# Kernel optimization log

Measured on AMD Instinct MI355X. Metric: run time of the kernel, lower is better.

## Reference

```python
import jax, jax.numpy as jnp
import numpy as np
from jax import lax

H = 512      # hidden_size (== embed dim)
K = 128      # attr_size
V = 32000    # output_size (vocab)
ANUM = 20    # aspect_num = len(aspect_ids)//100
N, B = 64, 32
T, S, A = 256, 32, 5


def setup_inputs() -> dict:
    key = jax.random.key(0)
    ks = jax.random.split(key, 32)
    f = lambda i, shape, s=0.02: (jax.random.normal(ks[i], shape, jnp.float32) * s)
    inp = {
        "input_seq": jax.random.randint(ks[0], (N, B), 0, V, jnp.int32),
        "last_hidden": jax.random.normal(ks[1], (1, B, H), jnp.float32),
        "encoder_out1": jax.random.normal(ks[2], (T, B, H), jnp.float32),
        "encoder_out2": jax.random.normal(ks[3], (S, B, H), jnp.float32),
        "encoder_out3": jax.random.normal(ks[4], (A, B, K), jnp.float32),
        "encoder_out4": jax.random.normal(ks[5], (A, B, ANUM), jnp.float32),
        "aspect_ids": jax.random.randint(ks[6], (100 * ANUM,), 0, V, jnp.int32),
        # learned parameters
        "emb": f(7, (V, H)),
        "gru_Wih": f(8, (3 * H, H)), "gru_Whh": f(9, (3 * H, H)),
        "gru_bih": f(10, (3 * H,)), "gru_bhh": f(11, (3 * H,)),
        "attn_W": f(12, (H, 2 * H)), "attn_b": f(13, (H,)), "attn_v": f(14, (H,)),
        "attr_W": f(15, (H, H + K)), "attr_b": f(16, (H,)), "attr_v": f(17, (H,)),
        "concat_W": f(18, (H, 3 * H + K)), "concat_b": f(19, (H,)),
        "out_W": f(20, (V, H)), "out_b": f(21, (V,)),
        "gate_W": f(22, (ANUM, 2 * H + ANUM)), "gate_b": f(23, (ANUM,)),
        "proj_W": f(24, (ANUM, 2 * ANUM)), "proj_b": f(25, (ANUM,)),
    }
    return inp


def _gru(x, h0, Wih, Whh, bih, bhh):
    # x: (N,B,H); h0: (B,H). PyTorch gate order: reset, update, new.
    def step(h, xt):
        gi = xt @ Wih.T + bih
        gh = h @ Whh.T + bhh
        ir, iz, inn = jnp.split(gi, 3, axis=-1)
        hr, hz, hn = jnp.split(gh, 3, axis=-1)
        r = jax.nn.sigmoid(ir + hr)
        z = jax.nn.sigmoid(iz + hz)
        n = jnp.tanh(inn + r * hn)
        h_new = (1.0 - z) * n + z * h
        return h_new, h_new
    hT, ys = lax.scan(step, h0, x)
    return ys, hT


def _attn(hidden, enc, W, b, v):
    # Faithful to Attn/AttributeAttn: energies[b,n,t] = tanh(v . (W @ cat(hidden[n,b], enc[t,b]) + b))
    # W @ cat = hidden @ Wh^T + enc @ We^T; dot with v distributes -> avoid (T,N,B,*) blowup.
    Hh = hidden.shape[-1]
    Wh, We = W[:, :Hh], W[:, Hh:]
    a = hidden @ (Wh.T @ v) + jnp.dot(b, v)   # (N,B)
    c = enc @ (We.T @ v)                       # (T,B)
    e = jnp.tanh(a.T[:, :, None] + c.T[:, None, :])  # (B,N,T)
    return jax.nn.softmax(e, axis=2)


def reference(input_seq, last_hidden, encoder_out1, encoder_out2, encoder_out3,
              encoder_out4, aspect_ids, emb, gru_Wih, gru_Whh, gru_bih, gru_bhh,
              attn_W, attn_b, attn_v, attr_W, attr_b, attr_v, concat_W, concat_b,
              out_W, out_b, gate_W, gate_b, proj_W, proj_b):
    seq_len = input_seq.shape[0]
    embedded = emb[input_seq]                                   # (N,B,H), dropout=eval noop
    rnn_output, hT = _gru(embedded, last_hidden[0], gru_Wih, gru_Whh, gru_bih, gru_bhh)
    hidden = hT[None]                                           # (1,B,H)

    aw1 = _attn(rnn_output, encoder_out1, attn_W, attn_b, attn_v)   # (B,N,T)
    ctx1 = jnp.einsum('bnt,tbh->nbh', aw1, encoder_out1)
    aw2 = _attn(rnn_output, encoder_out2, attn_W, attn_b, attn_v)   # (B,N,S)
    ctx2 = jnp.einsum('bns,sbh->nbh', aw2, encoder_out2)
    aw3 = _attn(rnn_output, encoder_out3, attr_W, attr_b, attr_v)   # (B,N,A)
    ctx3 = jnp.einsum('bna,abk->nbk', aw3, encoder_out3)

    concat_input = jnp.concatenate([rnn_output, ctx1, ctx2, ctx3], axis=2)
    concat_output = jnp.tanh(concat_input @ concat_W.T + concat_b)  # (N,B,H)
    output = concat_output @ out_W.T + out_b                        # (N,B,V)

    e4 = jnp.concatenate([encoder_out4[0], encoder_out4[1]], axis=-1)  # (B,2*ANUM)
    e4 = e4 @ proj_W.T + proj_b                                        # (B,ANUM)
    e4 = jnp.broadcast_to(e4[None], (seq_len,) + e4.shape)             # (N,B,ANUM)

    gate = jnp.tanh(jnp.concatenate([embedded, rnn_output, e4], axis=2) @ gate_W.T + gate_b)
    vals = jnp.tile(gate, (1, 1, 100))                                 # (N,B,100*ANUM)
    output = output.at[:, :, aspect_ids].add(vals)
    return output, hidden, aw1, aw2, aw3, gate
```

## Files before the change

### kernel.cpp

```cpp
#include <hip/hip_runtime.h>
#include <hip/hip_bf16.h>

#define HDIM 512
#define KA   128
#define VOC  32000
#define ANUMC 20
#define NSEQ 64
#define BATCH 32
#define TLEN 256
#define SLEN 32
#define ALEN 5
#define NB   2048
#define CIN  1664
#define G3H  1536
#define GB   64

typedef __bf16 bf16;
typedef bf16 v8bf __attribute__((ext_vector_type(8)));
typedef float v4f __attribute__((ext_vector_type(4)));

#define DEV __device__ __forceinline__

DEV float sigmoidf_(float x) { return 1.f / (1.f + expf(-x)); }

__global__ void k_tick(unsigned* ctr) {
  if (threadIdx.x == 0) ++*ctr;
}

__global__ void k_vec(const float* __restrict__ attn_W, const float* __restrict__ attn_b,
                      const float* __restrict__ attn_v,
                      const float* __restrict__ attr_W, const float* __restrict__ attr_b,
                      const float* __restrict__ attr_v,
                      const float* __restrict__ enc4, const float* __restrict__ pW,
                      const float* __restrict__ pb, float* __restrict__ misc) {
  int tid = threadIdx.x;
  int blk = blockIdx.x;
  if (blk == 0) {
    for (int i = tid; i < 512; i += 256) {
      float s = 0.f;
      for (int j = 0; j < 512; ++j) s += attn_W[j * 1024 + i] * attn_v[j];
      misc[i] = s;
    }
  } else if (blk == 1) {
    for (int i = tid; i < 512; i += 256) {
      float s = 0.f;
      for (int j = 0; j < 512; ++j) s += attn_W[j * 1024 + 512 + i] * attn_v[j];
      misc[512 + i] = s;
    }
  } else if (blk == 2) {
    for (int i = tid; i < 512; i += 256) {
      float s = 0.f;
      for (int j = 0; j < 512; ++j) s += attr_W[j * 640 + i] * attr_v[j];
      misc[1024 + i] = s;
    }
  } else {
    for (int i = tid; i < 128; i += 256) {
      float s = 0.f;
      for (int j = 0; j < 512; ++j) s += attr_W[j * 640 + 512 + i] * attr_v[j];
      misc[1536 + i] = s;
    }
    if (tid == 128) {
      float s = 0.f;
      for (int j = 0; j < 512; ++j) s += attn_b[j] * attn_v[j];
      misc[1664] = s;
    }
    if (tid == 129) {
      float s = 0.f;
      for (int j = 0; j < 512; ++j) s += attr_b[j] * attr_v[j];
      misc[1665] = s;
    }
    for (int i = tid; i < BATCH * ANUMC; i += 256) {
      int b = i / ANUMC, j = i % ANUMC;
      float s = pb[j];
      for (int q = 0; q < ANUMC; ++q) s += pW[j * 40 + q] * enc4[b * ANUMC + q];
      for (int q = 0; q < ANUMC; ++q) s += pW[j * 40 + 20 + q] * enc4[BATCH * ANUMC + b * ANUMC + q];
      misc[1792 + i] = s;
    }
  }
}

__global__ void k_embcvt(const int* __restrict__ seq, const float* __restrict__ emb,
                         float* __restrict__ embedded, bf16* __restrict__ emb_bf,
                         const float* __restrict__ Wih, bf16* __restrict__ Wih_bf,
                         const float* __restrict__ cW, bf16* __restrict__ cW_bf,
                         const float* __restrict__ oW, bf16* __restrict__ oW_bf) {
  size_t i = (size_t)blockIdx.x * 256 + threadIdx.x;
  const size_t s0 = 1048576, s1 = s0 + 786432, s2 = s1 + 851968, s3 = s2 + 16384000;
  if (i < s0) {
    int row = (int)(i >> 9), col = (int)(i & 511);
    float v = emb[(size_t)seq[row] * 512 + col];
    embedded[i] = v;
    emb_bf[i] = (bf16)v;
  } else if (i < s1) {
    size_t j = i - s0;
    Wih_bf[j] = (bf16)Wih[j];
  } else if (i < s2) {
    size_t j = i - s1;
    cW_bf[j] = (bf16)cW[j];
  } else if (i < s3) {
    size_t j = i - s2;
    oW_bf[j] = (bf16)oW[j];
  }
}

__global__ void k_c(const float* __restrict__ enc1, const float* __restrict__ enc2,
                    const float* __restrict__ enc3, float* __restrict__ misc) {
  int i = blockIdx.x * 256 + threadIdx.x;
  const float* u1e = misc + 512;
  const float* u3e = misc + 1536;
  if (i < 8192) {
    const float* row = enc1 + (size_t)i * 512;
    float s = 0.f;
#pragma unroll 4
    for (int j = 0; j < 512; j += 4) {
      float4 a = *(const float4*)(row + j);
      float4 u = *(const float4*)(u1e + j);
      s += a.x * u.x + a.y * u.y + a.z * u.z + a.w * u.w;
    }
    misc[2560 + i] = s;
  } else if (i < 8192 + 1024) {
    int k = i - 8192;
    const float* row = enc2 + (size_t)k * 512;
    float s = 0.f;
#pragma unroll 4
    for (int j = 0; j < 512; j += 4) {
      float4 a = *(const float4*)(row + j);
      float4 u = *(const float4*)(u1e + j);
      s += a.x * u.x + a.y * u.y + a.z * u.z + a.w * u.w;
    }
    misc[10752 + k] = s;
  } else if (i < 8192 + 1024 + 160) {
    int k = i - 9216;
    const float* row = enc3 + (size_t)k * 128;
    float s = 0.f;
#pragma unroll 4
    for (int j = 0; j < 128; j += 4) {
      float4 a = *(const float4*)(row + j);
      float4 u = *(const float4*)(u3e + j);
      s += a.x * u.x + a.y * u.y + a.z * u.z + a.w * u.w;
    }
    misc[11776 + k] = s;
  }
}

template <int EPI>
__global__ __launch_bounds__(256) void k_gemm_bt(const bf16* __restrict__ A,
                                                 const bf16* __restrict__ Bm,
                                                 const float* __restrict__ bias,
                                                 float* __restrict__ Cf, bf16* __restrict__ Cb,
                                                 int M, int Nn, int Kd) {
  __shared__ __align__(16) unsigned short As[128 * 64];
  __shared__ __align__(16) unsigned short Bs[128 * 64];
  int tid = threadIdx.x;
  int m0 = blockIdx.y * 128;
  int n0 = blockIdx.x * 128;
  int lane = tid & 63;
  int wv = tid >> 6;
  int wm = wv & 1, wn = wv >> 1;
  int l15 = lane & 15, quad = lane >> 4;
  int srow = tid >> 3;
  int sch = tid & 7;

  v4f acc[4][4];
#pragma unroll
  for (int i = 0; i < 4; ++i)
#pragma unroll
    for (int j = 0; j < 4; ++j) acc[i][j] = (v4f){0.f, 0.f, 0.f, 0.f};

  for (int kb = 0; kb < Kd; kb += 64) {
#pragma unroll
    for (int r = 0; r < 4; ++r) {
      int row = r * 32 + srow;
      uint4 va = *(const uint4*)(A + (size_t)(m0 + row) * Kd + kb + sch * 8);
      *(uint4*)((char*)As + row * 128 + ((sch ^ (row & 7)) << 4)) = va;
      uint4 vb = *(const uint4*)(Bm + (size_t)(n0 + row) * Kd + kb + sch * 8);
      *(uint4*)((char*)Bs + row * 128 + ((sch ^ (row & 7)) << 4)) = vb;
    }
    __syncthreads();
#pragma unroll
    for (int ks = 0; ks < 2; ++ks) {
      v8bf af[4], bfr[4];
      int c = ks * 4 + quad;
#pragma unroll
      for (int i = 0; i < 4; ++i) {
        int mr = wm * 64 + i * 16 + l15;
        af[i] = *(const v8bf*)((const char*)As + mr * 128 + ((c ^ (mr & 7)) << 4));
      }
#pragma unroll
      for (int j = 0; j < 4; ++j) {
        int nr = wn * 64 + j * 16 + l15;
        bfr[j] = *(const v8bf*)((const char*)Bs + nr * 128 + ((c ^ (nr & 7)) << 4));
      }
#pragma unroll
      for (int i = 0; i < 4; ++i)
#pragma unroll
        for (int j = 0; j < 4; ++j)
          acc[i][j] = __builtin_amdgcn_mfma_f32_16x16x32_bf16(af[i], bfr[j], acc[i][j], 0, 0, 0);
    }
    __syncthreads();
  }
#pragma unroll
  for (int i = 0; i < 4; ++i) {
    int gr0 = m0 + wm * 64 + i * 16 + quad * 4;
#pragma unroll
    for (int j = 0; j < 4; ++j) {
      int gc = n0 + wn * 64 + j * 16 + l15;
      float bs = bias[gc];
#pragma unroll
      for (int reg = 0; reg < 4; ++reg) {
        float v = acc[i][j][reg] + bs;
        if (EPI == 1)
          Cb[(size_t)(gr0 + reg) * Nn + gc] = (bf16)tanhf(v);
        else
          Cf[(size_t)(gr0 + reg) * Nn + gc] = v;
      }
    }
  }
}

__global__ __launch_bounds__(256) void k_gru(const float* __restrict__ gi,
                                             const float* __restrict__ Whh,
                                             const float* __restrict__ bhh,
                                             const float* __restrict__ lasth,
                                             float* __restrict__ rnn,
                                             bf16* __restrict__ concat_bf,
                                             unsigned long long* __restrict__ hx,
                                             const unsigned* __restrict__ ctr) {
  struct SMEM {
    unsigned short whh[24 * 512];
    unsigned short hs[32 * 512];
    float gh[32 * 29];
    unsigned short hnew[256];
  };
  __shared__ __align__(16) SMEM sm;
  int tid = threadIdx.x;
  int blk = blockIdx.x;
  int c0 = blk * 8;
  unsigned tagbase = (*ctr) << 6;

  for (int idx = tid; idx < 24 * 64; idx += 256) {
    int row = idx >> 6, cc = idx & 63;
    int g = row >> 3, jj = row & 7;
    const float* src = Whh + (size_t)(g * 512 + c0 + jj) * 512 + cc * 8;
    float4 x = *(const float4*)src;
    float4 y = *(const float4*)(src + 4);
    v8bf vv;
    vv[0] = (bf16)x.x; vv[1] = (bf16)x.y; vv[2] = (bf16)x.z; vv[3] = (bf16)x.w;
    vv[4] = (bf16)y.x; vv[5] = (bf16)y.y; vv[6] = (bf16)y.z; vv[7] = (bf16)y.w;
    *(v8bf*)((char*)sm.whh + row * 1024 + ((cc ^ (row & 7)) << 4)) = vv;
  }

  int lane = tid & 63;
  int w = tid >> 6;
  int l15 = lane & 15, quad = lane >> 4;
  int m0 = (w & 1) * 16;
  int n0 = (w >> 1) * 16;

  int cb = tid >> 3, j = tid & 7, c = c0 + j;
  float hprev = lasth[cb * 512 + c];
  float b_r = bhh[c], b_z = bhh[512 + c], b_n = bhh[1024 + c];

  for (int t = 0; t < 64; ++t) {
    const float* gii = gi + ((size_t)t * 32 + cb) * G3H;
    float g_r = gii[c];
    float g_z = gii[512 + c];
    float g_n = gii[1024 + c];

    if (t == 0) {
#pragma unroll
      for (int rnd = 0; rnd < 8; ++rnd) {
        int ch = rnd * 256 + tid;
        int bb = ch >> 6, cc = ch & 63;
        const float* hp = lasth + bb * 512 + cc * 8;
        float4 x = *(const float4*)hp;
        float4 y = *(const float4*)(hp + 4);
        v8bf vv;
        vv[0] = (bf16)x.x; vv[1] = (bf16)x.y; vv[2] = (bf16)x.z; vv[3] = (bf16)x.w;
        vv[4] = (bf16)y.x; vv[5] = (bf16)y.y; vv[6] = (bf16)y.z; vv[7] = (bf16)y.w;
        *(v8bf*)((char*)sm.hs + bb * 1024 + ((cc ^ (bb & 7)) << 4)) = vv;
      }
    } else {
      unsigned tg = tagbase + (unsigned)t;
      const unsigned long long* src = hx + (size_t)(t & 1) * 8192 + tid;
      unsigned long long v[32];
#pragma unroll
      for (int i = 0; i < 32; ++i)
        v[i] = __hip_atomic_load(src + i * 256, __ATOMIC_RELAXED, __HIP_MEMORY_SCOPE_AGENT);
      for (;;) {
        unsigned stale = 0u;
#pragma unroll
        for (int i = 0; i < 32; ++i)
          if ((unsigned)(v[i] >> 32) != tg) stale |= (1u << i);
        if (!stale) break;
        __builtin_amdgcn_s_sleep(1);
#pragma unroll
        for (int i = 0; i < 32; ++i)
          if (stale & (1u << i))
            v[i] = __hip_atomic_load(src + i * 256, __ATOMIC_RELAXED, __HIP_MEMORY_SCOPE_AGENT);
      }
      int cc = tid >> 2, b4 = (tid & 3) * 4;
#pragma unroll
      for (int i = 0; i < 32; ++i)
        *(unsigned*)((char*)sm.hs + i * 1024 + (((cc ^ (i & 7)) << 4) | b4)) = (unsigned)v[i];
    }
    __syncthreads();

    {
      v4f acc0 = (v4f){0.f, 0.f, 0.f, 0.f};
      v4f acc1 = (v4f){0.f, 0.f, 0.f, 0.f};
      int mr = m0 + l15;
      int nr = n0 + l15;
#pragma unroll
      for (int it = 0; it < 8; ++it) {
        {
          int ccx = it * 4 + quad;
          v8bf af = *(const v8bf*)((const char*)sm.hs + mr * 1024 + ((ccx ^ (mr & 7)) << 4));
          v8bf bfr = *(const v8bf*)((const char*)sm.whh + nr * 1024 + ((ccx ^ (nr & 7)) << 4));
          acc0 = __builtin_amdgcn_mfma_f32_16x16x32_bf16(af, bfr, acc0, 0, 0, 0);
        }
        {
          int ccx = (it + 8) * 4 + quad;
          v8bf af = *(const v8bf*)((const char*)sm.hs + mr * 1024 + ((ccx ^ (mr & 7)) << 4));
          v8bf bfr = *(const v8bf*)((const char*)sm.whh + nr * 1024 + ((ccx ^ (nr & 7)) << 4));
          acc1 = __builtin_amdgcn_mfma_f32_16x16x32_bf16(af, bfr, acc1, 0, 0, 0);
        }
      }
      v4f acc = acc0 + acc1;
      if (n0 == 0 || l15 < 8) {
#pragma unroll
        for (int reg = 0; reg < 4; ++reg)
          sm.gh[(m0 + quad * 4 + reg) * 29 + n0 + l15] = acc[reg];
      }
    }
    __syncthreads();

    {
      float ar = sm.gh[cb * 29 + j] + b_r;
      float az = sm.gh[cb * 29 + 8 + j] + b_z;
      float an = sm.gh[cb * 29 + 16 + j] + b_n;
      float rg = sigmoidf_(g_r + ar);
      float zg = sigmoidf_(g_z + az);
      float ng = tanhf(g_n + rg * an);
      float hn = (1.f - zg) * ng + zg * hprev;
      hprev = hn;
      rnn[((size_t)t * 32 + cb) * 512 + c] = hn;
      bf16 hb = (bf16)hn;
      concat_bf[((size_t)t * 32 + cb) * CIN + c] = hb;
      sm.hnew[tid] = *(unsigned short*)&hb;
    }

    if (t < 63) {
      __syncthreads();
      if (tid < 128) {
        int cbq = tid >> 2, wj = tid & 3;
        const unsigned short* hp = sm.hnew + cbq * 8 + wj * 2;
        unsigned long long pk = (unsigned long long)hp[0] |
                                ((unsigned long long)hp[1] << 16) |
                                ((unsigned long long)(tagbase + (unsigned)(t + 1)) << 32);
        __hip_atomic_store(hx + (size_t)((t + 1) & 1) * 8192 + cbq * 256 + blk * 4 + wj, pk,
                           __ATOMIC_RELAXED, __HIP_MEMORY_SCOPE_AGENT);
      }
    }
  }
}

__global__ __launch_bounds__(256) void k_attnrow(const float* __restrict__ rnn,
                                                 const float* __restrict__ misc,
                                                 float* __restrict__ aw1,
                                                 float* __restrict__ aw2,
                                                 float* __restrict__ aw3) {
  int wv = (blockIdx.x * 256 + threadIdx.x) >> 6;
  int lane = threadIdx.x & 63;
  if (wv >= 2048) return;
  int n = wv >> 5, b = wv & 31;
  const float* u1a = misc;
  const float* u3h = misc + 1024;
  const float* c1 = misc + 2560;
  const float* c2 = misc + 10752;
  const float* c3 = misc + 11776;
  const float* row = rnn + (size_t)(n * 32 + b) * 512;
  float s1 = 0.f, s3 = 0.f;
#pragma unroll
  for (int q = 0; q < 8; ++q) {
    int j = lane * 8 + q;
    float rv = row[j];
    s1 += rv * u1a[j];
    s3 += rv * u3h[j];
  }
  for (int o = 32; o > 0; o >>= 1) {
    s1 += __shfl_down(s1, o);
    s3 += __shfl_down(s3, o);
  }
  s1 = __shfl(s1, 0) + misc[1664];
  s3 = __shfl(s3, 0) + misc[1665];

  float e[4];
  float mx = -1e30f;
#pragma unroll
  for (int q = 0; q < 4; ++q) {
    int t = q * 64 + lane;
    e[q] = tanhf(s1 + c1[t * 32 + b]);
    mx = fmaxf(mx, e[q]);
  }
  for (int o = 32; o > 0; o >>= 1) mx = fmaxf(mx, __shfl_xor(mx, o));
  float sum = 0.f;
#pragma unroll
  for (int q = 0; q < 4; ++q) {
    e[q] = expf(e[q] - mx);
    sum += e[q];
  }
  for (int o = 32; o > 0; o >>= 1) sum += __shfl_xor(sum, o);
  float inv = 1.f / sum;
  size_t base1 = (size_t)(b * 64 + n) * 256;
#pragma unroll
  for (int q = 0; q < 4; ++q) aw1[base1 + q * 64 + lane] = e[q] * inv;

  float e2 = (lane < 32) ? tanhf(s1 + c2[lane * 32 + b]) : -1e30f;
  float m2 = e2;
  for (int o = 32; o > 0; o >>= 1) m2 = fmaxf(m2, __shfl_xor(m2, o));
  float x2 = (lane < 32) ? expf(e2 - m2) : 0.f;
  float sm2 = x2;
  for (int o = 32; o > 0; o >>= 1) sm2 += __shfl_xor(sm2, o);
  if (lane < 32) aw2[(size_t)(b * 64 + n) * 32 + lane] = x2 / sm2;

  float e3 = (lane < 5) ? tanhf(s3 + c3[lane * 32 + b]) : -1e30f;
  float m3 = e3;
  for (int o = 32; o > 0; o >>= 1) m3 = fmaxf(m3, __shfl_xor(m3, o));
  float x3 = (lane < 5) ? expf(e3 - m3) : 0.f;
  float sm3 = x3;
  for (int o = 32; o > 0; o >>= 1) sm3 += __shfl_xor(sm3, o);
  if (lane < 5) aw3[(size_t)(b * 64 + n) * 5 + lane] = x3 / sm3;
}

template <int TL, int COFF>
__global__ __launch_bounds__(256) void k_ctx(const float* __restrict__ aw,
                                             const float* __restrict__ enc,
                                             bf16* __restrict__ concat_bf) {
  __shared__ __align__(16) float awsT[TL * 36];
  int tid = threadIdx.x;
  int bx = blockIdx.x;
  int b = bx >> 2, q = (bx >> 1) & 1, nh = bx & 1;
  for (int i = tid; i < 32 * TL; i += 256) {
    int n = i / TL, te = i % TL;
    awsT[te * 36 + n] = aw[(size_t)b * 64 * TL + (size_t)(nh * 32 + n) * TL + te];
  }
  __syncthreads();
  int col = q * 256 + tid;
  float4 acc[8];
#pragma unroll
  for (int n4 = 0; n4 < 8; ++n4) acc[n4] = make_float4(0.f, 0.f, 0.f, 0.f);
  for (int te = 0; te < TL; ++te) {
    float v = enc[((size_t)te * 32 + b) * 512 + col];
#pragma unroll
    for (int n4 = 0; n4 < 8; ++n4) {
      float4 wv = *(const float4*)(awsT + te * 36 + n4 * 4);
      acc[n4].x += wv.x * v;
      acc[n4].y += wv.y * v;
      acc[n4].z += wv.z * v;
      acc[n4].w += wv.w * v;
    }
  }
#pragma unroll
  for (int n4 = 0; n4 < 8; ++n4) {
    int ng = nh * 32 + n4 * 4;
    concat_bf[((size_t)(ng + 0) * 32 + b) * CIN + COFF + col] = (bf16)acc[n4].x;
    concat_bf[((size_t)(ng + 1) * 32 + b) * CIN + COFF + col] = (bf16)acc[n4].y;
    concat_bf[((size_t)(ng + 2) * 32 + b) * CIN + COFF + col] = (bf16)acc[n4].z;
    concat_bf[((size_t)(ng + 3) * 32 + b) * CIN + COFF + col] = (bf16)acc[n4].w;
  }
}

__global__ void k_ctx3_misc(const float* __restrict__ aw3, const float* __restrict__ enc3,
                            const float* __restrict__ rnn, bf16* __restrict__ concat_bf,
                            float* __restrict__ hid) {
  int i = blockIdx.x * 256 + threadIdx.x;
  if (i < NB * 128) {
    int row = i >> 7, k = i & 127;
    int n = row >> 5, b = row & 31;
    float s = 0.f;
#pragma unroll
    for (int a = 0; a < 5; ++a)
      s += aw3[(size_t)(b * 64 + n) * 5 + a] * enc3[((size_t)a * 32 + b) * 128 + k];
    concat_bf[(size_t)row * CIN + 1536 + k] = (bf16)s;
  } else {
    int j = i - NB * 128;
    if (j < 16384) hid[j] = rnn[(size_t)63 * 16384 + j];
  }
}

__global__ __launch_bounds__(256) void k_gate(const float* __restrict__ embedded,
                                              const float* __restrict__ rnn,
                                              const float* __restrict__ misc,
                                              const float* __restrict__ gW,
                                              const float* __restrict__ gb,
                                              float* __restrict__ gate) {
  int i = blockIdx.x * 256 + threadIdx.x;
  if (i >= NB * ANUMC) return;
  int row = i / ANUMC, j = i % ANUMC;
  int b = row & 31;
  const float* w = gW + (size_t)j * 1044;
  const float* e = embedded + (size_t)row * 512;
  const float* r = rnn + (size_t)row * 512;
  float s = gb[j];
#pragma unroll 4
  for (int k = 0; k < 512; k += 4) {
    float4 a = *(const float4*)(e + k);
    float4 ww = *(const float4*)(w + k);
    s += a.x * ww.x + a.y * ww.y + a.z * ww.z + a.w * ww.w;
  }
#pragma unroll 4
  for (int k = 0; k < 512; k += 4) {
    float4 a = *(const float4*)(r + k);
    float4 ww = *(const float4*)(w + 512 + k);
    s += a.x * ww.x + a.y * ww.y + a.z * ww.z + a.w * ww.w;
  }
  const float* e4 = misc + 1792 + b * ANUMC;
#pragma unroll
  for (int q = 0; q < ANUMC; ++q) s += w[1024 + q] * e4[q];
  gate[i] = tanhf(s);
}

__global__ __launch_bounds__(256) void k_aspect(const int* __restrict__ ids,
                                                const float* __restrict__ gate,
                                                float* __restrict__ out) {
  __shared__ float gs[ANUMC];
  int row = blockIdx.x;
  if (threadIdx.x < ANUMC) gs[threadIdx.x] = gate[(size_t)row * ANUMC + threadIdx.x];
  __syncthreads();
  float* orow = out + (size_t)row * VOC;
  for (int k = threadIdx.x; k < 2000; k += 256) {
    atomicAdd(orow + ids[k], gs[k % ANUMC]);
  }
}

extern "C" void kernel_launch(void* const* d_in, const int* in_sizes, int n_in,
                              void* d_out, int out_size, void* d_ws, size_t ws_size,
                              hipStream_t stream) {
  const int* seq = (const int*)d_in[0];
  const float* lasth = (const float*)d_in[1];
  const float* enc1 = (const float*)d_in[2];
  const float* enc2 = (const float*)d_in[3];
  const float* enc3 = (const float*)d_in[4];
  const float* enc4 = (const float*)d_in[5];
  const int* aspect = (const int*)d_in[6];
  const float* emb = (const float*)d_in[7];
  const float* Wih = (const float*)d_in[8];
  const float* Whh = (const float*)d_in[9];
  const float* bih = (const float*)d_in[10];
  const float* bhh = (const float*)d_in[11];
  const float* attn_W = (const float*)d_in[12];
  const float* attn_b = (const float*)d_in[13];
  const float* attn_v = (const float*)d_in[14];
  const float* attr_W = (const float*)d_in[15];
  const float* attr_b = (const float*)d_in[16];
  const float* attr_v = (const float*)d_in[17];
  const float* cW = (const float*)d_in[18];
  const float* cbias = (const float*)d_in[19];
  const float* oW = (const float*)d_in[20];
  const float* ob = (const float*)d_in[21];
  const float* gW = (const float*)d_in[22];
  const float* gb = (const float*)d_in[23];
  const float* pW = (const float*)d_in[24];
  const float* pb = (const float*)d_in[25];

  char* ws = (char*)d_ws;
  float* misc = (float*)(ws + 0);
  float* embedded = (float*)(ws + 65536);
  float* gi = (float*)(ws + 4259840);
  float* rnn = (float*)(ws + 16842752);
  bf16* emb_bf = (bf16*)(ws + 21037056);
  bf16* Wih_bf = (bf16*)(ws + 23134208);
  bf16* cW_bf = (bf16*)(ws + 24707072);
  bf16* oW_bf = (bf16*)(ws + 26411008);
  bf16* concat_bf = (bf16*)(ws + 59179008);
  bf16* cout_bf = (bf16*)(ws + 65994752);
  unsigned long long* hx = (unsigned long long*)(ws + 68091904);
  unsigned* ctr = (unsigned*)(misc + 12032);

  float* out = (float*)d_out;
  float* hid_out = out + 65536000;
  float* aw1 = out + 65552384;
  float* aw2 = out + 66076672;
  float* aw3 = out + 66142208;
  float* gate = out + 66152448;

  k_tick<<<1, 64, 0, stream>>>(ctr);
  k_vec<<<4, 256, 0, stream>>>(attn_W, attn_b, attn_v, attr_W, attr_b, attr_v, enc4, pW, pb, misc);
  k_embcvt<<<74496, 256, 0, stream>>>(seq, emb, embedded, emb_bf, Wih, Wih_bf, cW, cW_bf, oW,
                                      oW_bf);
  k_c<<<37, 256, 0, stream>>>(enc1, enc2, enc3, misc);
  k_gemm_bt<0><<<dim3(12, 16), 256, 0, stream>>>(emb_bf, Wih_bf, bih, gi, nullptr, NB, G3H, 512);
  k_gru<<<GB, 256, 0, stream>>>(gi, Whh, bhh, lasth, rnn, concat_bf, hx, ctr);
  k_attnrow<<<512, 256, 0, stream>>>(rnn, misc, aw1, aw2, aw3);
  k_ctx<256, 512><<<128, 256, 0, stream>>>(aw1, enc1, concat_bf);
  k_ctx<32, 1024><<<128, 256, 0, stream>>>(aw2, enc2, concat_bf);
  k_ctx3_misc<<<1088, 256, 0, stream>>>(aw3, enc3, rnn, concat_bf, hid_out);
  k_gate<<<160, 256, 0, stream>>>(embedded, rnn, misc, gW, gb, gate);
  k_gemm_bt<1><<<dim3(4, 16), 256, 0, stream>>>(concat_bf, cW_bf, cbias, nullptr, cout_bf, NB,
                                                512, CIN);
  k_gemm_bt<0><<<dim3(250, 16), 256, 0, stream>>>(cout_bf, oW_bf, ob, out, nullptr, NB, VOC, 512);
  k_aspect<<<2048, 256, 0, stream>>>(aspect, gate, out);
}
```

Baseline: 1.232 ms.

## Fuse aspect scatter into output GEMM epilogue and rework GRU sync

```diff
diff --git a/kernel.cpp b/kernel.cpp
--- a/kernel.cpp
+++ b/kernel.cpp
@@ -23,8 +23,21 @@
 
 DEV float sigmoidf_(float x) { return 1.f / (1.f + expf(-x)); }
 
-__global__ void k_tick(unsigned* ctr) {
-  if (threadIdx.x == 0) ++*ctr;
+__global__ void k_zero(int* bar) {
+  for (int i = threadIdx.x; i < GB * 32; i += 256) bar[i] = 0;
+}
+
+__global__ void k_init0(float* addtab, int* colnz) {
+  int i = blockIdx.x * 256 + threadIdx.x;
+  if (i < VOC * ANUMC) addtab[i] = 0.f;
+  if (i < VOC) colnz[i] = 0;
+}
+__global__ void k_init1(const int* __restrict__ ids, float* addtab, int* colnz) {
+  for (int k = threadIdx.x; k < 2000; k += 256) {
+    int j = ids[k];
+    atomicAdd(addtab + (size_t)j * ANUMC + (k % ANUMC), 1.0f);
+    colnz[j] = 1;
+  }
 }
 
 __global__ void k_vec(const float* __restrict__ attn_W, const float* __restrict__ attn_b,
@@ -148,7 +161,10 @@
                                                  const bf16* __restrict__ Bm,
                                                  const float* __restrict__ bias,
                                                  float* __restrict__ Cf, bf16* __restrict__ Cb,
-                                                 int M, int Nn, int Kd) {
+                                                 int M, int Nn, int Kd,
+                                                 const float* __restrict__ addtab,
+                                                 const int* __restrict__ colnz,
+                                                 const float* __restrict__ gate) {
   __shared__ __align__(16) unsigned short As[128 * 64];
   __shared__ __align__(16) unsigned short Bs[128 * 64];
   int tid = threadIdx.x;
@@ -206,13 +222,32 @@
     for (int j = 0; j < 4; ++j) {
       int gc = n0 + wn * 64 + j * 16 + l15;
       float bs = bias[gc];
-#pragma unroll
-      for (int reg = 0; reg < 4; ++reg) {
-        float v = acc[i][j][reg] + bs;
-        if (EPI == 1)
-          Cb[(size_t)(gr0 + reg) * Nn + gc] = (bf16)tanhf(v);
-        else
+      if (EPI == 2) {
+        int nz = colnz[gc];
+        float ar[ANUMC];
+        if (nz) {
+#pragma unroll
+          for (int a = 0; a < ANUMC; ++a) ar[a] = addtab[(size_t)gc * ANUMC + a];
+        }
+#pragma unroll
+        for (int reg = 0; reg < 4; ++reg) {
+          float v = acc[i][j][reg] + bs;
+          if (nz) {
+            const float* gr = gate + (size_t)(gr0 + reg) * ANUMC;
+#pragma unroll
+            for (int a = 0; a < ANUMC; ++a) v += ar[a] * gr[a];
+          }
           Cf[(size_t)(gr0 + reg) * Nn + gc] = v;
+        }
+      } else {
+#pragma unroll
+        for (int reg = 0; reg < 4; ++reg) {
+          float v = acc[i][j][reg] + bs;
+          if (EPI == 1)
+            Cb[(size_t)(gr0 + reg) * Nn + gc] = (bf16)tanhf(v);
+          else
+            Cf[(size_t)(gr0 + reg) * Nn + gc] = v;
+        }
       }
     }
   }
@@ -225,30 +260,17 @@
                                              float* __restrict__ rnn,
                                              bf16* __restrict__ concat_bf,
                                              unsigned long long* __restrict__ hx,
-                                             const unsigned* __restrict__ ctr) {
+                                             int* __restrict__ bar) {
   struct SMEM {
-    unsigned short whh[24 * 512];
     unsigned short hs[32 * 512];
     float gh[32 * 29];
     unsigned short hnew[256];
+    int go;
   };
   __shared__ __align__(16) SMEM sm;
   int tid = threadIdx.x;
   int blk = blockIdx.x;
   int c0 = blk * 8;
-  unsigned tagbase = (*ctr) << 6;
-
-  for (int idx = tid; idx < 24 * 64; idx += 256) {
-    int row = idx >> 6, cc = idx & 63;
-    int g = row >> 3, jj = row & 7;
-    const float* src = Whh + (size_t)(g * 512 + c0 + jj) * 512 + cc * 8;
-    float4 x = *(const float4*)src;
-    float4 y = *(const float4*)(src + 4);
-    v8bf vv;
-    vv[0] = (bf16)x.x; vv[1] = (bf16)x.y; vv[2] = (bf16)x.z; vv[3] = (bf16)x.w;
-    vv[4] = (bf16)y.x; vv[5] = (bf16)y.y; vv[6] = (bf16)y.z; vv[7] = (bf16)y.w;
-    *(v8bf*)((char*)sm.whh + row * 1024 + ((cc ^ (row & 7)) << 4)) = vv;
-  }
 
   int lane = tid & 63;
   int w = tid >> 6;
@@ -256,9 +278,42 @@
   int m0 = (w & 1) * 16;
   int n0 = (w >> 1) * 16;
 
+  if (tid == 0) sm.go = 0;
+
+  v8bf breg[16];
+  {
+    int nr = n0 + l15;
+    if (nr > 23) nr = 23;
+    const float* wrow = Whh + (size_t)((nr >> 3) * 512 + c0 + (nr & 7)) * 512;
+#pragma unroll
+    for (int it = 0; it < 16; ++it) {
+      int k0 = it * 32 + quad * 8;
+      float4 x = *(const float4*)(wrow + k0);
+      float4 y = *(const float4*)(wrow + k0 + 4);
+      v8bf vv;
+      vv[0] = (bf16)x.x; vv[1] = (bf16)x.y; vv[2] = (bf16)x.z; vv[3] = (bf16)x.w;
+      vv[4] = (bf16)y.x; vv[5] = (bf16)y.y; vv[6] = (bf16)y.z; vv[7] = (bf16)y.w;
+      breg[it] = vv;
+    }
+  }
+
+#pragma unroll
+  for (int rnd = 0; rnd < 8; ++rnd) {
+    int ch = rnd * 256 + tid;
+    int bb = ch >> 6, cc = ch & 63;
+    const float* hp = lasth + bb * 512 + cc * 8;
+    float4 x = *(const float4*)hp;
+    float4 y = *(const float4*)(hp + 4);
+    v8bf vv;
+    vv[0] = (bf16)x.x; vv[1] = (bf16)x.y; vv[2] = (bf16)x.z; vv[3] = (bf16)x.w;
+    vv[4] = (bf16)y.x; vv[5] = (bf16)y.y; vv[6] = (bf16)y.z; vv[7] = (bf16)y.w;
+    *(v8bf*)((char*)sm.hs + bb * 1024 + ((cc ^ (bb & 7)) << 4)) = vv;
+  }
+
   int cb = tid >> 3, j = tid & 7, c = c0 + j;
   float hprev = lasth[cb * 512 + c];
   float b_r = bhh[c], b_z = bhh[512 + c], b_n = bhh[1024 + c];
+  __syncthreads();
 
   for (int t = 0; t < 64; ++t) {
     const float* gii = gi + ((size_t)t * 32 + cb) * G3H;
@@ -266,63 +321,21 @@
     float g_z = gii[512 + c];
     float g_n = gii[1024 + c];
 
-    if (t == 0) {
-#pragma unroll
-      for (int rnd = 0; rnd < 8; ++rnd) {
-        int ch = rnd * 256 + tid;
-        int bb = ch >> 6, cc = ch & 63;
-        const float* hp = lasth + bb * 512 + cc * 8;
-        float4 x = *(const float4*)hp;
-        float4 y = *(const float4*)(hp + 4);
-        v8bf vv;
-        vv[0] = (bf16)x.x; vv[1] = (bf16)x.y; vv[2] = (bf16)x.z; vv[3] = (bf16)x.w;
-        vv[4] = (bf16)y.x; vv[5] = (bf16)y.y; vv[6] = (bf16)y.z; vv[7] = (bf16)y.w;
-        *(v8bf*)((char*)sm.hs + bb * 1024 + ((cc ^ (bb & 7)) << 4)) = vv;
-      }
-    } else {
-      unsigned tg = tagbase + (unsigned)t;
-      const unsigned long long* src = hx + (size_t)(t & 1) * 8192 + tid;
-      unsigned long long v[32];
-#pragma unroll
-      for (int i = 0; i < 32; ++i)
-        v[i] = __hip_atomic_load(src + i * 256, __ATOMIC_RELAXED, __HIP_MEMORY_SCOPE_AGENT);
-      for (;;) {
-        unsigned stale = 0u;
-#pragma unroll
-        for (int i = 0; i < 32; ++i)
-          if ((unsigned)(v[i] >> 32) != tg) stale |= (1u << i);
-        if (!stale) break;
-        __builtin_amdgcn_s_sleep(1);
-#pragma unroll
-        for (int i = 0; i < 32; ++i)
-          if (stale & (1u << i))
-            v[i] = __hip_atomic_load(src + i * 256, __ATOMIC_RELAXED, __HIP_MEMORY_SCOPE_AGENT);
-      }
-      int cc = tid >> 2, b4 = (tid & 3) * 4;
-#pragma unroll
-      for (int i = 0; i < 32; ++i)
-        *(unsigned*)((char*)sm.hs + i * 1024 + (((cc ^ (i & 7)) << 4) | b4)) = (unsigned)v[i];
-    }
-    __syncthreads();
-
     {
       v4f acc0 = (v4f){0.f, 0.f, 0.f, 0.f};
       v4f acc1 = (v4f){0.f, 0.f, 0.f, 0.f};
       int mr = m0 + l15;
-      int nr = n0 + l15;
 #pragma unroll
       for (int it = 0; it < 8; ++it) {
         {
           int ccx = it * 4 + quad;
           v8bf af = *(const v8bf*)((const char*)sm.hs + mr * 1024 + ((ccx ^ (mr & 7)) << 4));
-          v8bf bfr = *(const v8bf*)((const char*)sm.whh + nr * 1024 + ((ccx ^ (nr & 7)) << 4));
-          acc0 = __builtin_amdgcn_mfma_f32_16x16x32_bf16(af, bfr, acc0, 0, 0, 0);
+          acc0 = __builtin_amdgcn_mfma_f32_16x16x32_bf16(af, breg[it], acc0, 0, 0, 0);
         }
         {
           int ccx = (it + 8) * 4 + quad;
           v8bf af = *(const v8bf*)((const char*)sm.hs + mr * 1024 + ((ccx ^ (mr & 7)) << 4));
-          v8bf bfr = *(const v8bf*)((const char*)sm.whh + nr * 1024 + ((ccx ^ (nr & 7)) << 4));
-          acc1 = __builtin_amdgcn_mfma_f32_16x16x32_bf16(af, bfr, acc1, 0, 0, 0);
+          acc1 = __builtin_amdgcn_mfma_f32_16x16x32_bf16(af, breg[it + 8], acc1, 0, 0, 0);
         }
       }
       v4f acc = acc0 + acc1;
@@ -351,15 +364,45 @@
 
     if (t < 63) {
       __syncthreads();
-      if (tid < 128) {
-        int cbq = tid >> 2, wj = tid & 3;
-        const unsigned short* hp = sm.hnew + cbq * 8 + wj * 2;
-        unsigned long long pk = (unsigned long long)hp[0] |
-                                ((unsigned long long)hp[1] << 16) |
-                                ((unsigned long long)(tagbase + (unsigned)(t + 1)) << 32);
-        __hip_atomic_store(hx + (size_t)((t + 1) & 1) * 8192 + cbq * 256 + blk * 4 + wj, pk,
+      int target = t + 1;
+      int pnext = target & 1;
+      if (w == 0) {
+        unsigned long long pk = *(const unsigned long long*)(sm.hnew + lane * 4);
+        int wd = (lane >> 1) * 128 + blk * 2 + (lane & 1);
+        __hip_atomic_store(hx + (size_t)pnext * 4096 + wd, pk,
                            __ATOMIC_RELAXED, __HIP_MEMORY_SCOPE_AGENT);
+        asm volatile("s_waitcnt vmcnt(0)" ::: "memory");
+        if (lane == 0)
+          __hip_atomic_store(&bar[blk * 32], target, __ATOMIC_RELAXED,
+                             __HIP_MEMORY_SCOPE_AGENT);
+        for (;;) {
+          int v = __hip_atomic_load(&bar[lane * 32], __ATOMIC_RELAXED,
+                                    __HIP_MEMORY_SCOPE_AGENT);
+          if (__all(v >= target)) break;
+          __builtin_amdgcn_s_sleep(1);
+        }
+        if (lane == 0) *(volatile int*)&sm.go = target;
+      } else {
+        while (*(volatile int*)&sm.go < target) __builtin_amdgcn_s_sleep(1);
       }
+
+      {
+        const unsigned long long* src = hx + (size_t)pnext * 4096 + w * 1024 + lane;
+        unsigned long long vv[16];
+#pragma unroll
+        for (int i = 0; i < 16; ++i)
+          vv[i] = __hip_atomic_load(src + i * 64, __ATOMIC_RELAXED,
+                                    __HIP_MEMORY_SCOPE_AGENT);
+#pragma unroll
+        for (int i = 0; i < 16; ++i) {
+          int W = w * 1024 + i * 64 + lane;
+          int bb = W >> 7, wr = W & 127;
+          int u = wr >> 1, half = wr & 1;
+          *(unsigned long long*)((char*)sm.hs + bb * 1024 +
+                                 (((u ^ (bb & 7)) << 4) | (half << 3))) = vv[i];
+        }
+      }
+      __syncthreads();
     }
   }
 }
@@ -518,19 +561,6 @@
 #pragma unroll
   for (int q = 0; q < ANUMC; ++q) s += w[1024 + q] * e4[q];
   gate[i] = tanhf(s);
-}
-
-__global__ __launch_bounds__(256) void k_aspect(const int* __restrict__ ids,
-                                                const float* __restrict__ gate,
-                                                float* __restrict__ out) {
-  __shared__ float gs[ANUMC];
-  int row = blockIdx.x;
-  if (threadIdx.x < ANUMC) gs[threadIdx.x] = gate[(size_t)row * ANUMC + threadIdx.x];
-  __syncthreads();
-  float* orow = out + (size_t)row * VOC;
-  for (int k = threadIdx.x; k < 2000; k += 256) {
-    atomicAdd(orow + ids[k], gs[k % ANUMC]);
-  }
 }
 
 extern "C" void kernel_launch(void* const* d_in, const int* in_sizes, int n_in,
@@ -575,7 +605,9 @@
   bf16* concat_bf = (bf16*)(ws + 59179008);
   bf16* cout_bf = (bf16*)(ws + 65994752);
   unsigned long long* hx = (unsigned long long*)(ws + 68091904);
-  unsigned* ctr = (unsigned*)(misc + 12032);
+  int* bar = (int*)(misc + 12032);
+  float* addtab = (float*)(ws + 4259840);
+  int* colnz = (int*)(ws + 4259840 + 2560000);
 
   float* out = (float*)d_out;
   float* hid_out = out + 65536000;
@@ -584,20 +616,23 @@
   float* aw3 = out + 66142208;
   float* gate = out + 66152448;
 
-  k_tick<<<1, 64, 0, stream>>>(ctr);
+  k_zero<<<1, 256, 0, stream>>>(bar);
   k_vec<<<4, 256, 0, stream>>>(attn_W, attn_b, attn_v, attr_W, attr_b, attr_v, enc4, pW, pb, misc);
   k_embcvt<<<74496, 256, 0, stream>>>(seq, emb, embedded, emb_bf, Wih, Wih_bf, cW, cW_bf, oW,
                                       oW_bf);
   k_c<<<37, 256, 0, stream>>>(enc1, enc2, enc3, misc);
-  k_gemm_bt<0><<<dim3(12, 16), 256, 0, stream>>>(emb_bf, Wih_bf, bih, gi, nullptr, NB, G3H, 512);
-  k_gru<<<GB, 256, 0, stream>>>(gi, Whh, bhh, lasth, rnn, concat_bf, hx, ctr);
+  k_gemm_bt<0><<<dim3(12, 16), 256, 0, stream>>>(emb_bf, Wih_bf, bih, gi, nullptr, NB, G3H, 512,
+                                                 nullptr, nullptr, nullptr);
+  k_gru<<<GB, 256, 0, stream>>>(gi, Whh, bhh, lasth, rnn, concat_bf, hx, bar);
+  k_init0<<<2625, 256, 0, stream>>>(addtab, colnz);
+  k_init1<<<1, 256, 0, stream>>>(aspect, addtab, colnz);
   k_attnrow<<<512, 256, 0, stream>>>(rnn, misc, aw1, aw2, aw3);
   k_ctx<256, 512><<<128, 256, 0, stream>>>(aw1, enc1, concat_bf);
   k_ctx<32, 1024><<<128, 256, 0, stream>>>(aw2, enc2, concat_bf);
   k_ctx3_misc<<<1088, 256, 0, stream>>>(aw3, enc3, rnn, concat_bf, hid_out);
   k_gate<<<160, 256, 0, stream>>>(embedded, rnn, misc, gW, gb, gate);
   k_gemm_bt<1><<<dim3(4, 16), 256, 0, stream>>>(concat_bf, cW_bf, cbias, nullptr, cout_bf, NB,
-                                                512, CIN);
-  k_gemm_bt<0><<<dim3(250, 16), 256, 0, stream>>>(cout_bf, oW_bf, ob, out, nullptr, NB, VOC, 512);
-  k_aspect<<<2048, 256, 0, stream>>>(aspect, gate, out);
-}
+                                                512, CIN, nullptr, nullptr, nullptr);
+  k_gemm_bt<2><<<dim3(250, 16), 256, 0, stream>>>(cout_bf, oW_bf, ob, out, nullptr, NB, VOC, 512,
+                                                  addtab, colnz, gate);
+}
```

Result: faster. 1.089 ms (-11.6%).
